# Performance work log

Hardware: AMD Instinct MI355X
Metric: run time of the kernel (lower is better)

Reference implementation:

```python
import jax, jax.numpy as jnp
import numpy as np

B, S, D, H = 4, 1024, 1024, 16
HD = D // H  # head_dim = 64


def setup_inputs() -> dict:
    key = jax.random.key(0)
    ks = jax.random.split(key, 16)
    w = lambda k: jax.random.normal(k, (D, D), dtype=jnp.float32) * 0.02
    b = lambda k: jax.random.normal(k, (D,), dtype=jnp.float32) * 0.02
    x = jax.random.normal(ks[0], (B, S, D), dtype=jnp.float32)
    mask = jnp.tril(jnp.ones((S, S), dtype=jnp.int32))[None, None]  # causal [1,1,S,S]
    bar_indices = jax.random.randint(ks[1], (S,), 0, S, dtype=jnp.int64)
    beat_indices = jax.random.randint(ks[2], (S,), 0, S, dtype=jnp.int64)
    return {
        "x": x, "mask": mask, "bar_indices": bar_indices, "beat_indices": beat_indices,
        "Wq": w(ks[3]), "bq": b(ks[4]), "Wk": w(ks[5]), "bk": b(ks[6]),
        "Wv": w(ks[7]), "bv": b(ks[8]),
        "W_bark": w(ks[9]), "b_bark": b(ks[10]),
        "W_beatk": w(ks[11]), "b_beatk": b(ks[12]),
        "Wo": w(ks[13]), "bo": b(ks[14]),
    }


def reference(x, mask, bar_indices, beat_indices, Wq, bq, Wk, bk, Wv, bv,
              W_bark, b_bark, W_beatk, b_beatk, Wo, bo):
    Bs, Sl, Dm = x.shape
    heads, hd = H, Dm // H

    def proj(t, W, b):  # torch Linear: t @ W.T + b, then split heads -> [B,H,S,hd]
        y = t @ W.T + b
        return y.reshape(Bs, -1, heads, hd).transpose(0, 2, 1, 3)

    q = proj(x, Wq, bq)
    k = proj(x, Wk, bk)
    v = proj(x, Wv, bv)
    scale = 1.0 / jnp.sqrt(jnp.asarray(hd, x.dtype))

    scores = jnp.einsum('bhqd,bhkd->bhqk', q, k) * scale

    # hierarchical bar bias (bar_query is computed but unused in the original)
    bar_k = proj(x[:, bar_indices], W_bark, b_bark)
    scores = scores + 0.2 * (jnp.einsum('bhqd,bhkd->bhqk', q, bar_k) * scale)

    # hierarchical beat bias
    beat_k = proj(x[:, beat_indices], W_beatk, b_beatk)
    scores = scores + 0.1 * (jnp.einsum('bhqd,bhkd->bhqk', q, beat_k) * scale)

    scores = jnp.where(mask == 0, jnp.asarray(-1e9, scores.dtype), scores)
    attn = jax.nn.softmax(scores, axis=-1)  # dropout is identity in eval

    out = jnp.einsum('bhqk,bhkd->bhqd', attn, v)
    out = out.transpose(0, 2, 1, 3).reshape(Bs, Sl, Dm)
    return out @ Wo.T + bo
```

## Files before the change

kernel.cpp:

```cpp
#include <hip/hip_runtime.h>
#include <hip/hip_bf16.h>


typedef __bf16 bf16x8 __attribute__((ext_vector_type(8)));
typedef __bf16 bf16x4 __attribute__((ext_vector_type(4)));
typedef float  f32x4  __attribute__((ext_vector_type(4)));

#define DMODEL 1024

#define ASYNC_LOAD16(gp, lp)                                                  \
    __builtin_amdgcn_global_load_lds(                                         \
        (const __attribute__((address_space(1))) unsigned int*)(gp),          \
        (__attribute__((address_space(3))) unsigned int*)(lp), 16, 0, 0)

__global__ __launch_bounds__(256) void cvt_kernel(
    const float* __restrict__ x,
    const float* __restrict__ Wq, const float* __restrict__ Wk,
    const float* __restrict__ Wv, const float* __restrict__ Wbar,
    const float* __restrict__ Wbeat, const float* __restrict__ Wo,
    __bf16* __restrict__ dst)
{
    const int g = blockIdx.x * 256 + threadIdx.x;
    const size_t e = (size_t)g * 8;
    const int seg = (int)(e >> 20);
    const float* src; size_t off; float s = 1.0f;
    if (seg < 4)       { src = x;     off = e; }
    else if (seg == 4) { src = Wq;    off = e - ((size_t)4 << 20); }
    else if (seg == 5) { src = Wk;    off = e - ((size_t)5 << 20); }
    else if (seg == 6) { src = Wv;    off = e - ((size_t)6 << 20); }
    else if (seg == 7) { src = Wbar;  off = e - ((size_t)7 << 20); s = 0.2f; }
    else if (seg == 8) { src = Wbeat; off = e - ((size_t)8 << 20); s = 0.1f; }
    else               { src = Wo;    off = e - ((size_t)9 << 20); }
    const float4 a = *(const float4*)&src[off];
    const float4 b = *(const float4*)&src[off + 4];
    bf16x8 v;
    v[0] = (__bf16)(a.x * s); v[1] = (__bf16)(a.y * s);
    v[2] = (__bf16)(a.z * s); v[3] = (__bf16)(a.w * s);
    v[4] = (__bf16)(b.x * s); v[5] = (__bf16)(b.y * s);
    v[6] = (__bf16)(b.z * s); v[7] = (__bf16)(b.w * s);
    *(bf16x8*)&dst[e] = v;
}

__global__ __launch_bounds__(256) void proj_kernel(
    const __bf16* __restrict__ xb, const __bf16* __restrict__ attnbuf,
    const __bf16* __restrict__ Wqb, const __bf16* __restrict__ Wkb,
    const __bf16* __restrict__ Wvb, const __bf16* __restrict__ Wbarb,
    const __bf16* __restrict__ Wbeatb, const __bf16* __restrict__ Wob,
    const float* __restrict__ bq, const float* __restrict__ bk,
    const float* __restrict__ bv, const float* __restrict__ bbar,
    const float* __restrict__ bbeat, const float* __restrict__ bo,
    const int* __restrict__ bar_idx, const int* __restrict__ beat_idx,
    __bf16* __restrict__ qbuf, __bf16* __restrict__ keffbuf,
    __bf16* __restrict__ vtbuf, float* __restrict__ outbuf,
    int mode_base)
{
    const int mode = mode_base + blockIdx.y;
    const int tile = blockIdx.x;
    const int m0 = (tile >> 3) << 7;
    const int n0 = (tile & 7) << 7;

    __shared__ __align__(16) __bf16 Alds[128 * 32];
    __shared__ __align__(16) __bf16 Blds[128 * 32];

    const int t    = threadIdx.x;
    const int w    = t >> 6;
    const int lane = t & 63;
    const int l15  = lane & 15;
    const int quad = lane >> 4;
    const int wm   = (w >> 1) << 6;
    const int wn   = (w & 1) << 6;
    const int srow = t >> 2;
    const int scol = (t & 3) * 8;

    const __bf16* Aptr = (mode == 3) ? attnbuf : xb;
    const int nterms = (mode == 1) ? 3 : 1;

    f32x4 acc[4][4];
    for (int i = 0; i < 4; ++i)
        for (int j = 0; j < 4; ++j)
            acc[i][j] = {0.f, 0.f, 0.f, 0.f};

    for (int term = 0; term < nterms; ++term) {
        const __bf16* Wterm =
            (mode == 0) ? Wqb :
            (mode == 2) ? Wvb :
            (mode == 3) ? Wob :
            (term == 0) ? Wkb : (term == 1) ? Wbarb : Wbeatb;

        int arow0, arow1;
        if (mode != 1 || term == 0) {
            arow0 = m0 + srow;
            arow1 = m0 + 64 + srow;
        } else {
            const int* gi = (term == 1) ? bar_idx : beat_idx;
            const int bbase = m0 & ~1023;
            arow0 = bbase + gi[(m0 & 1023) + srow];
            arow1 = bbase + gi[(m0 & 1023) + 64 + srow];
        }
        const __bf16* gA0 = Aptr + (size_t)arow0 * DMODEL + scol;
        const __bf16* gA1 = Aptr + (size_t)arow1 * DMODEL + scol;
        const __bf16* gB0 = Wterm + (size_t)(n0 + srow) * DMODEL + scol;
        const __bf16* gB1 = Wterm + (size_t)(n0 + 64 + srow) * DMODEL + scol;
        __bf16* lA0 = &Alds[w * 512];
        __bf16* lA1 = &Alds[2048 + w * 512];
        __bf16* lB0 = &Blds[w * 512];
        __bf16* lB1 = &Blds[2048 + w * 512];

        for (int kk = 0; kk < 32; ++kk) {
            const int k0 = kk * 32;
            ASYNC_LOAD16(gA0 + k0, lA0);
            ASYNC_LOAD16(gA1 + k0, lA1);
            ASYNC_LOAD16(gB0 + k0, lB0);
            ASYNC_LOAD16(gB1 + k0, lB1);
            __syncthreads();

            bf16x8 af[4], bfr[4];
            for (int i = 0; i < 4; ++i)
                af[i] = *(const bf16x8*)&Alds[(wm + i * 16 + l15) * 32 + quad * 8];
            for (int j = 0; j < 4; ++j)
                bfr[j] = *(const bf16x8*)&Blds[(wn + j * 16 + l15) * 32 + quad * 8];

            for (int i = 0; i < 4; ++i)
                for (int j = 0; j < 4; ++j)
                    acc[i][j] = __builtin_amdgcn_mfma_f32_16x16x32_bf16(
                        af[i], bfr[j], acc[i][j], 0, 0, 0);
            __syncthreads();
        }
    }

    for (int j = 0; j < 4; ++j) {
        const int col = n0 + wn + j * 16 + l15;
        float bias;
        if (mode == 0)      bias = bq[col];
        else if (mode == 1) bias = bk[col] + 0.2f * bbar[col] + 0.1f * bbeat[col];
        else if (mode == 2) bias = bv[col];
        else                bias = bo[col];

        for (int i = 0; i < 4; ++i) {
            const int rowbase = m0 + wm + i * 16 + quad * 4;
            if (mode == 2) {
                const int bb = rowbase >> 10;
                const int sb = rowbase & 1023;
                bf16x4 vv;
                for (int r = 0; r < 4; ++r) vv[r] = (__bf16)(acc[i][j][r] + bias);
                *(bf16x4*)&vtbuf[((size_t)(bb * 1024 + col)) * 1024 + sb] = vv;
            } else if (mode == 3) {
                for (int r = 0; r < 4; ++r)
                    outbuf[(size_t)(rowbase + r) * DMODEL + col] =
                        acc[i][j][r] + bias;
            } else if (mode == 0) {
                for (int r = 0; r < 4; ++r)
                    qbuf[(size_t)(rowbase + r) * DMODEL + col] =
                        (__bf16)((acc[i][j][r] + bias) * 0.125f);
            } else {
                for (int r = 0; r < 4; ++r)
                    keffbuf[(size_t)(rowbase + r) * DMODEL + col] =
                        (__bf16)(acc[i][j][r] + bias);
            }
        }
    }
}

__global__ __launch_bounds__(256) void oproj_kernel(
    const __bf16* __restrict__ attnb, const __bf16* __restrict__ Wob,
    const float* __restrict__ bo, float* __restrict__ outb)
{
    const int tile = blockIdx.x;
    const int m0 = (tile >> 3) << 6;
    const int n0 = (tile & 7) << 7;

    __shared__ __align__(16) __bf16 Alds[64 * 32];
    __shared__ __align__(16) __bf16 Blds[128 * 32];

    const int t    = threadIdx.x;
    const int w    = t >> 6;
    const int lane = t & 63;
    const int l15  = lane & 15;
    const int quad = lane >> 4;
    const int wm   = (w >> 1) << 5;
    const int wn   = (w & 1) << 6;
    const int srow = t >> 2;
    const int scol = (t & 3) * 8;

    const __bf16* gA  = attnb + (size_t)(m0 + srow) * DMODEL + scol;
    const __bf16* gB0 = Wob + (size_t)(n0 + srow) * DMODEL + scol;
    const __bf16* gB1 = Wob + (size_t)(n0 + 64 + srow) * DMODEL + scol;
    __bf16* lA  = &Alds[w * 512];
    __bf16* lB0 = &Blds[w * 512];
    __bf16* lB1 = &Blds[2048 + w * 512];

    f32x4 acc[2][4];
    for (int i = 0; i < 2; ++i)
        for (int j = 0; j < 4; ++j)
            acc[i][j] = {0.f, 0.f, 0.f, 0.f};

    for (int kk = 0; kk < 32; ++kk) {
        const int k0 = kk * 32;
        ASYNC_LOAD16(gA + k0, lA);
        ASYNC_LOAD16(gB0 + k0, lB0);
        ASYNC_LOAD16(gB1 + k0, lB1);
        __syncthreads();

        bf16x8 af[2], bfr[4];
        for (int i = 0; i < 2; ++i)
            af[i] = *(const bf16x8*)&Alds[(wm + i * 16 + l15) * 32 + quad * 8];
        for (int j = 0; j < 4; ++j)
            bfr[j] = *(const bf16x8*)&Blds[(wn + j * 16 + l15) * 32 + quad * 8];

        for (int i = 0; i < 2; ++i)
            for (int j = 0; j < 4; ++j)
                acc[i][j] = __builtin_amdgcn_mfma_f32_16x16x32_bf16(
                    af[i], bfr[j], acc[i][j], 0, 0, 0);
        __syncthreads();
    }

    for (int j = 0; j < 4; ++j) {
        const int col = n0 + wn + j * 16 + l15;
        const float bias = bo[col];
        for (int i = 0; i < 2; ++i) {
            const int rowbase = m0 + wm + i * 16 + quad * 4;
            for (int r = 0; r < 4; ++r)
                outb[(size_t)(rowbase + r) * DMODEL + col] = acc[i][j][r] + bias;
        }
    }
}

__global__ __launch_bounds__(256) void attn_kernel(
    const __bf16* __restrict__ qbuf, const __bf16* __restrict__ keffbuf,
    const __bf16* __restrict__ vtbuf, __bf16* __restrict__ attnbuf)
{
    const int bh = blockIdx.y;
    const int b  = bh >> 4;
    const int h  = bh & 15;
    const int qt = blockIdx.x;
    const int q0 = qt * 64;

    __shared__ __align__(16) __bf16 Klds[64][72];
    __shared__ __align__(16) __bf16 Vlds[64][72];
    __shared__ __align__(16) __bf16 Plds[4][16][72];

    const int t    = threadIdx.x;
    const int w    = t >> 6;
    const int lane = t & 63;
    const int l15  = lane & 15;
    const int quad = lane >> 4;

    const __bf16* qbase =
        qbuf + (size_t)(b * 1024 + q0 + w * 16 + l15) * DMODEL + h * 64;
    bf16x8 qf0 = *(const bf16x8*)&qbase[quad * 8];
    bf16x8 qf1 = *(const bf16x8*)&qbase[32 + quad * 8];

    bf16x8 ones;
    for (int i = 0; i < 8; ++i) ones[i] = (__bf16)1.0f;

    f32x4 o[4];
    for (int i = 0; i < 4; ++i) o[i] = {0.f, 0.f, 0.f, 0.f};
    f32x4 lacc = {0.f, 0.f, 0.f, 0.f};

    const int srow = t >> 2;
    const int scol = (t & 3) * 16;

    const __bf16* kbase = keffbuf + (size_t)(b * 1024) * DMODEL + h * 64;
    const __bf16* vtb   = vtbuf + (size_t)(b * 1024 + h * 64) * 1024;

    for (int j = 0; j <= qt; ++j) {
        const __bf16* kg = kbase + (size_t)(j * 64 + srow) * DMODEL + scol;
        *(bf16x8*)&Klds[srow][scol]     = *(const bf16x8*)kg;
        *(bf16x8*)&Klds[srow][scol + 8] = *(const bf16x8*)(kg + 8);
        const __bf16* vg = vtb + (size_t)srow * 1024 + j * 64 + scol;
        *(bf16x8*)&Vlds[srow][scol]     = *(const bf16x8*)vg;
        *(bf16x8*)&Vlds[srow][scol + 8] = *(const bf16x8*)(vg + 8);
        __syncthreads();

        f32x4 sc[4];
        for (int nt = 0; nt < 4; ++nt) {
            sc[nt] = {0.f, 0.f, 0.f, 0.f};
            bf16x8 kf0 = *(const bf16x8*)&Klds[nt * 16 + l15][quad * 8];
            bf16x8 kf1 = *(const bf16x8*)&Klds[nt * 16 + l15][32 + quad * 8];
            sc[nt] = __builtin_amdgcn_mfma_f32_16x16x32_bf16(qf0, kf0, sc[nt], 0, 0, 0);
            sc[nt] = __builtin_amdgcn_mfma_f32_16x16x32_bf16(qf1, kf1, sc[nt], 0, 0, 0);
        }

        if (j == qt) {
            const int qrow_base = q0 + w * 16 + quad * 4;
            for (int nt = 0; nt < 4; ++nt) {
                const int kcol = j * 64 + nt * 16 + l15;
                for (int r = 0; r < 4; ++r)
                    if (kcol > qrow_base + r) sc[nt][r] = -1e30f;
            }
        }

        for (int nt = 0; nt < 4; ++nt)
            for (int r = 0; r < 4; ++r)
                sc[nt][r] = __expf(sc[nt][r]);

        for (int nt = 0; nt < 4; ++nt)
            for (int r = 0; r < 4; ++r)
                Plds[w][quad * 4 + r][nt * 16 + l15] = (__bf16)sc[nt][r];
        asm volatile("s_waitcnt lgkmcnt(0)" ::: "memory");

        bf16x8 pf0 = *(const bf16x8*)&Plds[w][l15][quad * 8];
        bf16x8 pf1 = *(const bf16x8*)&Plds[w][l15][32 + quad * 8];

        lacc = __builtin_amdgcn_mfma_f32_16x16x32_bf16(pf0, ones, lacc, 0, 0, 0);
        lacc = __builtin_amdgcn_mfma_f32_16x16x32_bf16(pf1, ones, lacc, 0, 0, 0);

        for (int nd = 0; nd < 4; ++nd) {
            bf16x8 vf0 = *(const bf16x8*)&Vlds[nd * 16 + l15][quad * 8];
            bf16x8 vf1 = *(const bf16x8*)&Vlds[nd * 16 + l15][32 + quad * 8];
            o[nd] = __builtin_amdgcn_mfma_f32_16x16x32_bf16(pf0, vf0, o[nd], 0, 0, 0);
            o[nd] = __builtin_amdgcn_mfma_f32_16x16x32_bf16(pf1, vf1, o[nd], 0, 0, 0);
        }
        __syncthreads();
    }

    float rinv[4];
    for (int r = 0; r < 4; ++r) rinv[r] = 1.0f / lacc[r];
    for (int nd = 0; nd < 4; ++nd) {
        for (int r = 0; r < 4; ++r) {
            const int row = q0 + w * 16 + quad * 4 + r;
            attnbuf[(size_t)(b * 1024 + row) * DMODEL + h * 64 + nd * 16 + l15] =
                (__bf16)(o[nd][r] * rinv[r]);
        }
    }
}

extern "C" void kernel_launch(void* const* d_in, const int* in_sizes, int n_in,
                              void* d_out, int out_size, void* d_ws, size_t ws_size,
                              hipStream_t stream) {
    const float* x     = (const float*)d_in[0];
    const int* bar     = (const int*)d_in[2];
    const int* beat    = (const int*)d_in[3];
    const float* Wq    = (const float*)d_in[4];
    const float* bq    = (const float*)d_in[5];
    const float* Wk    = (const float*)d_in[6];
    const float* bk    = (const float*)d_in[7];
    const float* Wv    = (const float*)d_in[8];
    const float* bv    = (const float*)d_in[9];
    const float* Wbar  = (const float*)d_in[10];
    const float* bbar  = (const float*)d_in[11];
    const float* Wbeat = (const float*)d_in[12];
    const float* bbeat = (const float*)d_in[13];
    const float* Wo    = (const float*)d_in[14];
    const float* bo    = (const float*)d_in[15];

    const size_t M1 = (size_t)1 << 20;
    __bf16* xb     = (__bf16*)d_ws;
    __bf16* Wqb    = xb + 4 * M1;
    __bf16* Wkb    = Wqb + M1;
    __bf16* Wvb    = Wkb + M1;
    __bf16* Wbarb  = Wvb + M1;
    __bf16* Wbeatb = Wbarb + M1;
    __bf16* Wob    = Wbeatb + M1;
    __bf16* qbuf   = Wob + M1;
    __bf16* keff   = qbuf + 4 * M1;
    __bf16* vt     = keff + 4 * M1;
    __bf16* attn   = vt + 4 * M1;
    float*  outb   = (float*)d_out;

    cvt_kernel<<<5120, 256, 0, stream>>>(x, Wq, Wk, Wv, Wbar, Wbeat, Wo, xb);

    proj_kernel<<<dim3(256, 3), 256, 0, stream>>>(
        xb, attn, Wqb, Wkb, Wvb, Wbarb, Wbeatb, Wob,
        bq, bk, bv, bbar, bbeat, bo, bar, beat,
        qbuf, keff, vt, outb, 0);

    attn_kernel<<<dim3(16, 64), 256, 0, stream>>>(qbuf, keff, vt, attn);

    oproj_kernel<<<512, 256, 0, stream>>>(attn, Wob, bo, outb);
}
```

Measured before the change: 236.6 us.

## Pair causal query tiles per block and load K/V fragments directly

Each attention block now handles two query tiles, k and 15-k, so every block does the same causal work and the triangular imbalance goes away. Both tiles share the K and V fragments. Those fragments are read straight from global memory into registers, with no LDS staging and no __syncthreads. This halves the grid to 512 blocks and raises register pressure, and each wave now loads K/V directly from global memory, relying on the caches instead of shared memory.

Result: slower. 250.1 us (+5.7%).

```diff
diff --git a/kernel.cpp b/kernel.cpp
--- a/kernel.cpp
+++ b/kernel.cpp
@@ -229,15 +229,15 @@
     const __bf16* __restrict__ qbuf, const __bf16* __restrict__ keffbuf,
     const __bf16* __restrict__ vtbuf, __bf16* __restrict__ attnbuf)
 {
-    const int bh = blockIdx.y;
+    const int bh = blockIdx.x;
     const int b  = bh >> 4;
     const int h  = bh & 15;
-    const int qt = blockIdx.x;
-    const int q0 = qt * 64;
-
-    __shared__ __align__(16) __bf16 Klds[64][72];
-    __shared__ __align__(16) __bf16 Vlds[64][72];
-    __shared__ __align__(16) __bf16 Plds[4][16][72];
+    const int k  = blockIdx.y;
+    const int qA = k * 64;
+    const int qB = (15 - k) * 64;
+
+    __shared__ __align__(16) __bf16 PldsA[4][16][72];
+    __shared__ __align__(16) __bf16 PldsB[4][16][72];
 
     const int t    = threadIdx.x;
     const int w    = t >> 6;
@@ -245,82 +245,121 @@
     const int l15  = lane & 15;
     const int quad = lane >> 4;
 
-    const __bf16* qbase =
-        qbuf + (size_t)(b * 1024 + q0 + w * 16 + l15) * DMODEL + h * 64;
-    bf16x8 qf0 = *(const bf16x8*)&qbase[quad * 8];
-    bf16x8 qf1 = *(const bf16x8*)&qbase[32 + quad * 8];
+    const __bf16* qbA =
+        qbuf + (size_t)(b * 1024 + qA + w * 16 + l15) * DMODEL + h * 64;
+    const __bf16* qbB =
+        qbuf + (size_t)(b * 1024 + qB + w * 16 + l15) * DMODEL + h * 64;
+    bf16x8 qfA0 = *(const bf16x8*)&qbA[quad * 8];
+    bf16x8 qfA1 = *(const bf16x8*)&qbA[32 + quad * 8];
+    bf16x8 qfB0 = *(const bf16x8*)&qbB[quad * 8];
+    bf16x8 qfB1 = *(const bf16x8*)&qbB[32 + quad * 8];
 
     bf16x8 ones;
     for (int i = 0; i < 8; ++i) ones[i] = (__bf16)1.0f;
 
-    f32x4 o[4];
-    for (int i = 0; i < 4; ++i) o[i] = {0.f, 0.f, 0.f, 0.f};
-    f32x4 lacc = {0.f, 0.f, 0.f, 0.f};
-
-    const int srow = t >> 2;
-    const int scol = (t & 3) * 16;
-
-    const __bf16* kbase = keffbuf + (size_t)(b * 1024) * DMODEL + h * 64;
-    const __bf16* vtb   = vtbuf + (size_t)(b * 1024 + h * 64) * 1024;
-
-    for (int j = 0; j <= qt; ++j) {
-        const __bf16* kg = kbase + (size_t)(j * 64 + srow) * DMODEL + scol;
-        *(bf16x8*)&Klds[srow][scol]     = *(const bf16x8*)kg;
-        *(bf16x8*)&Klds[srow][scol + 8] = *(const bf16x8*)(kg + 8);
-        const __bf16* vg = vtb + (size_t)srow * 1024 + j * 64 + scol;
-        *(bf16x8*)&Vlds[srow][scol]     = *(const bf16x8*)vg;
-        *(bf16x8*)&Vlds[srow][scol + 8] = *(const bf16x8*)(vg + 8);
-        __syncthreads();
-
-        f32x4 sc[4];
+    f32x4 oA[4], oB[4];
+    for (int i = 0; i < 4; ++i) { oA[i] = {0.f,0.f,0.f,0.f}; oB[i] = {0.f,0.f,0.f,0.f}; }
+    f32x4 laccA = {0.f, 0.f, 0.f, 0.f};
+    f32x4 laccB = {0.f, 0.f, 0.f, 0.f};
+
+    const __bf16* kb = keffbuf + (size_t)(b * 1024) * DMODEL + h * 64;
+    const __bf16* vb = vtbuf + (size_t)(b * 1024 + h * 64) * 1024;
+
+    const int jend = 15 - k;
+    for (int j = 0; j <= jend; ++j) {
+        const bool dual = (j <= k);
+
+        bf16x8 kf[4][2];
         for (int nt = 0; nt < 4; ++nt) {
-            sc[nt] = {0.f, 0.f, 0.f, 0.f};
-            bf16x8 kf0 = *(const bf16x8*)&Klds[nt * 16 + l15][quad * 8];
-            bf16x8 kf1 = *(const bf16x8*)&Klds[nt * 16 + l15][32 + quad * 8];
-            sc[nt] = __builtin_amdgcn_mfma_f32_16x16x32_bf16(qf0, kf0, sc[nt], 0, 0, 0);
-            sc[nt] = __builtin_amdgcn_mfma_f32_16x16x32_bf16(qf1, kf1, sc[nt], 0, 0, 0);
-        }
-
-        if (j == qt) {
-            const int qrow_base = q0 + w * 16 + quad * 4;
+            const __bf16* kr = kb + (size_t)(j * 64 + nt * 16 + l15) * DMODEL;
+            kf[nt][0] = *(const bf16x8*)&kr[quad * 8];
+            kf[nt][1] = *(const bf16x8*)&kr[32 + quad * 8];
+        }
+
+        f32x4 sB[4], sA[4];
+        for (int nt = 0; nt < 4; ++nt) {
+            sB[nt] = {0.f, 0.f, 0.f, 0.f};
+            sB[nt] = __builtin_amdgcn_mfma_f32_16x16x32_bf16(qfB0, kf[nt][0], sB[nt], 0, 0, 0);
+            sB[nt] = __builtin_amdgcn_mfma_f32_16x16x32_bf16(qfB1, kf[nt][1], sB[nt], 0, 0, 0);
+        }
+        if (dual) {
+            for (int nt = 0; nt < 4; ++nt) {
+                sA[nt] = {0.f, 0.f, 0.f, 0.f};
+                sA[nt] = __builtin_amdgcn_mfma_f32_16x16x32_bf16(qfA0, kf[nt][0], sA[nt], 0, 0, 0);
+                sA[nt] = __builtin_amdgcn_mfma_f32_16x16x32_bf16(qfA1, kf[nt][1], sA[nt], 0, 0, 0);
+            }
+        }
+
+        if (j == jend) {
+            const int rb = qB + w * 16 + quad * 4;
             for (int nt = 0; nt < 4; ++nt) {
                 const int kcol = j * 64 + nt * 16 + l15;
                 for (int r = 0; r < 4; ++r)
-                    if (kcol > qrow_base + r) sc[nt][r] = -1e30f;
+                    if (kcol > rb + r) sB[nt][r] = -1e30f;
+            }
+        }
+        if (dual && j == k) {
+            const int ra = qA + w * 16 + quad * 4;
+            for (int nt = 0; nt < 4; ++nt) {
+                const int kcol = j * 64 + nt * 16 + l15;
+                for (int r = 0; r < 4; ++r)
+                    if (kcol > ra + r) sA[nt][r] = -1e30f;
             }
         }
 
         for (int nt = 0; nt < 4; ++nt)
             for (int r = 0; r < 4; ++r)
-                sc[nt][r] = __expf(sc[nt][r]);
+                sB[nt][r] = __expf(sB[nt][r]);
+        if (dual)
+            for (int nt = 0; nt < 4; ++nt)
+                for (int r = 0; r < 4; ++r)
+                    sA[nt][r] = __expf(sA[nt][r]);
+
+        bf16x8 vf[4][2];
+        for (int nd = 0; nd < 4; ++nd) {
+            const __bf16* vr = vb + (size_t)(nd * 16 + l15) * 1024 + j * 64;
+            vf[nd][0] = *(const bf16x8*)&vr[quad * 8];
+            vf[nd][1] = *(const bf16x8*)&vr[32 + quad * 8];
+        }
 
         for (int nt = 0; nt < 4; ++nt)
             for (int r = 0; r < 4; ++r)
-                Plds[w][quad * 4 + r][nt * 16 + l15] = (__bf16)sc[nt][r];
+                PldsB[w][quad * 4 + r][nt * 16 + l15] = (__bf16)sB[nt][r];
+        if (dual)
+            for (int nt = 0; nt < 4; ++nt)
+                for (int r = 0; r < 4; ++r)
+                    PldsA[w][quad * 4 + r][nt * 16 + l15] = (__bf16)sA[nt][r];
         asm volatile("s_waitcnt lgkmcnt(0)" ::: "memory");
 
-        bf16x8 pf0 = *(const bf16x8*)&Plds[w][l15][quad * 8];
-        bf16x8 pf1 = *(const bf16x8*)&Plds[w][l15][32 + quad * 8];
-
-        lacc = __builtin_amdgcn_mfma_f32_16x16x32_bf16(pf0, ones, lacc, 0, 0, 0);
-        lacc = __builtin_amdgcn_mfma_f32_16x16x32_bf16(pf1, ones, lacc, 0, 0, 0);
-
+        bf16x8 pfB0 = *(const bf16x8*)&PldsB[w][l15][quad * 8];
+        bf16x8 pfB1 = *(const bf16x8*)&PldsB[w][l15][32 + quad * 8];
+        laccB = __builtin_amdgcn_mfma_f32_16x16x32_bf16(pfB0, ones, laccB, 0, 0, 0);
+        laccB = __builtin_amdgcn_mfma_f32_16x16x32_bf16(pfB1, ones, laccB, 0, 0, 0);
         for (int nd = 0; nd < 4; ++nd) {
-            bf16x8 vf0 = *(const bf16x8*)&Vlds[nd * 16 + l15][quad * 8];
-            bf16x8 vf1 = *(const bf16x8*)&Vlds[nd * 16 + l15][32 + quad * 8];
-            o[nd] = __builtin_amdgcn_mfma_f32_16x16x32_bf16(pf0, vf0, o[nd], 0, 0, 0);
-            o[nd] = __builtin_amdgcn_mfma_f32_16x16x32_bf16(pf1, vf1, o[nd], 0, 0, 0);
-        }
-        __syncthreads();
-    }
-
-    float rinv[4];
-    for (int r = 0; r < 4; ++r) rinv[r] = 1.0f / lacc[r];
+            oB[nd] = __builtin_amdgcn_mfma_f32_16x16x32_bf16(pfB0, vf[nd][0], oB[nd], 0, 0, 0);
+            oB[nd] = __builtin_amdgcn_mfma_f32_16x16x32_bf16(pfB1, vf[nd][1], oB[nd], 0, 0, 0);
+        }
+        if (dual) {
+            bf16x8 pfA0 = *(const bf16x8*)&PldsA[w][l15][quad * 8];
+            bf16x8 pfA1 = *(const bf16x8*)&PldsA[w][l15][32 + quad * 8];
+            laccA = __builtin_amdgcn_mfma_f32_16x16x32_bf16(pfA0, ones, laccA, 0, 0, 0);
+            laccA = __builtin_amdgcn_mfma_f32_16x16x32_bf16(pfA1, ones, laccA, 0, 0, 0);
+            for (int nd = 0; nd < 4; ++nd) {
+                oA[nd] = __builtin_amdgcn_mfma_f32_16x16x32_bf16(pfA0, vf[nd][0], oA[nd], 0, 0, 0);
+                oA[nd] = __builtin_amdgcn_mfma_f32_16x16x32_bf16(pfA1, vf[nd][1], oA[nd], 0, 0, 0);
+            }
+        }
+    }
+
+    float rinvA[4], rinvB[4];
+    for (int r = 0; r < 4; ++r) { rinvA[r] = 1.0f / laccA[r]; rinvB[r] = 1.0f / laccB[r]; }
     for (int nd = 0; nd < 4; ++nd) {
         for (int r = 0; r < 4; ++r) {
-            const int row = q0 + w * 16 + quad * 4 + r;
-            attnbuf[(size_t)(b * 1024 + row) * DMODEL + h * 64 + nd * 16 + l15] =
-                (__bf16)(o[nd][r] * rinv[r]);
+            const int rowA = qA + w * 16 + quad * 4 + r;
+            const int rowB = qB + w * 16 + quad * 4 + r;
+            const int col  = h * 64 + nd * 16 + l15;
+            attnbuf[(size_t)(b * 1024 + rowA) * DMODEL + col] = (__bf16)(oA[nd][r] * rinvA[r]);
+            attnbuf[(size_t)(b * 1024 + rowB) * DMODEL + col] = (__bf16)(oB[nd][r] * rinvB[r]);
         }
     }
 }
@@ -365,7 +404,7 @@
         bq, bk, bv, bbar, bbeat, bo, bar, beat,
         qbuf, keff, vt, outb, 0);
 
-    attn_kernel<<<dim3(16, 64), 256, 0, stream>>>(qbuf, keff, vt, attn);
+    attn_kernel<<<dim3(64, 8), 256, 0, stream>>>(qbuf, keff, vt, attn);
 
     oproj_kernel<<<512, 256, 0, stream>>>(attn, Wob, bo, outb);
 }
```
